# Optimization experiments

Hardware: AMD Instinct MI355X
Metric: run time of the kernel (lower is better)

Reference implementation:

```python
import jax, jax.numpy as jnp
import numpy as np

B, S, H, NH = 2, 2048, 2048, 16
HD = H // NH


def setup_inputs() -> dict:
    key = jax.random.key(0)
    ks = jax.random.split(key, 9)
    s = 1.0 / np.sqrt(H)
    return {
        "hidden_state": jax.random.normal(ks[0], (B, S, H), dtype=jnp.float32),
        "Wq": jax.random.normal(ks[1], (H, H), dtype=jnp.float32) * s,
        "bq": jnp.zeros((H,), dtype=jnp.float32),
        "Wk": jax.random.normal(ks[2], (H, H), dtype=jnp.float32) * s,
        "bk": jnp.zeros((H,), dtype=jnp.float32),
        "Wv": jax.random.normal(ks[3], (H, H), dtype=jnp.float32) * s,
        "bv": jnp.zeros((H,), dtype=jnp.float32),
        "Wo": jax.random.normal(ks[4], (H, H), dtype=jnp.float32) * s,
        "bo": jnp.zeros((H,), dtype=jnp.float32),
    }


def _split_heads(x):
    # [B,S,H] -> [B,NH,S,HD]
    b, s, _ = x.shape
    return x.reshape(b, s, NH, HD).transpose(0, 2, 1, 3)


def reference(hidden_state, Wq, bq, Wk, bk, Wv, bv, Wo, bo):
    q = _split_heads(hidden_state @ Wq.T + bq)
    k = _split_heads(hidden_state @ Wk.T + bk)
    v = _split_heads(hidden_state @ Wv.T + bv)
    scale = 1.0 / jnp.sqrt(jnp.array(HD, dtype=q.dtype))
    scores = jnp.einsum("bhqd,bhkd->bhqk", q, k) * scale
    attn = jax.nn.softmax(scores, axis=-1)
    out = jnp.einsum("bhqk,bhkd->bhqd", attn, v)  # [B,NH,S,HD]
    out = out.transpose(0, 2, 1, 3).reshape(hidden_state.shape[0], -1, H)
    return out @ Wo.T + bo
```

## Files before the change

### kernel.cpp

```cpp
#include <hip/hip_runtime.h>
#include <hip/hip_bf16.h>
#include <stdint.h>

#define B_ 2
#define S_ 2048
#define H_ 2048
#define NH_ 16
#define HD_ 128
#define M_ (B_*S_)

typedef __attribute__((ext_vector_type(8))) short short8_t;
typedef __attribute__((ext_vector_type(4))) float floatx4;
typedef __attribute__((ext_vector_type(16))) float floatx16;

__device__ __forceinline__ short f2bf(float f) {
  union { float f; uint32_t u; } x; x.f = f;
  const uint32_t u = x.u;
  return (short)((u + 0x7FFFu + ((u >> 16) & 1u)) >> 16);
}

__device__ __forceinline__ void gload_lds16(const void* g, void* l) {
  __builtin_amdgcn_global_load_lds(
      (const __attribute__((address_space(1))) void*)g,
      (__attribute__((address_space(3))) void*)l, 16, 0, 0);
}

__global__ __launch_bounds__(256)
void cast_all(const float* __restrict__ h,  const float* __restrict__ wq,
              const float* __restrict__ wk, const float* __restrict__ wv,
              const float* __restrict__ wo,
              short* __restrict__ hB,  short* __restrict__ wqB,
              short* __restrict__ wkB, short* __restrict__ wvB,
              short* __restrict__ woB) {
  const int blk = blockIdx.x;
  const float* src; short* dst; int off;
  if      (blk <  4096) { src = h;  dst = hB;  off = blk; }
  else if (blk <  6144) { src = wq; dst = wqB; off = blk - 4096; }
  else if (blk <  8192) { src = wk; dst = wkB; off = blk - 6144; }
  else if (blk < 10240) { src = wv; dst = wvB; off = blk - 8192; }
  else                  { src = wo; dst = woB; off = blk - 10240; }
  const int i = (off * 256 + threadIdx.x) * 8;
  typedef __attribute__((ext_vector_type(4))) float f4;
  const f4 a = *(const f4*)(src + i);
  const f4 b = *(const f4*)(src + i + 4);
  short8_t o;
  o[0] = f2bf(a[0]); o[1] = f2bf(a[1]); o[2] = f2bf(a[2]); o[3] = f2bf(a[3]);
  o[4] = f2bf(b[0]); o[5] = f2bf(b[1]); o[6] = f2bf(b[2]); o[7] = f2bf(b[3]);
  *(short8_t*)(dst + i) = o;
}

template<int MODE>
__device__ __forceinline__
void gemm_body(const short* __restrict__ A, const short* __restrict__ Bm,
               const float* __restrict__ bias, void* __restrict__ C,
               const int m0, const int n0, const int N, const int K) {
  __shared__ short As[128 * 64];
  __shared__ short Bs[128 * 64];
  const int tid = threadIdx.x;
  const int wv = tid >> 6, ln = tid & 63;
  const int lr = ln >> 4, lc = ln & 15;
  const int wm = (wv >> 1) * 64, wn = (wv & 1) * 64;
  const int srow = ln >> 3;
  const int sc   = (ln & 7) ^ srow;

  floatx4 acc[4][4] = {};
  const short* aP[4];
  const short* bP[4];
#pragma unroll
  for (int i = 0; i < 4; ++i)
    aP[i] = A + (size_t)(m0 + wv * 32 + i * 8 + srow) * K + sc * 8;
#pragma unroll
  for (int i = 0; i < 4; ++i)
    bP[i] = Bm + (size_t)(n0 + wv * 32 + i * 8 + srow) * K + sc * 8;
  const int sw = (lc & 7) << 3;

  for (int k0 = 0; k0 < K; k0 += 64) {
#pragma unroll
    for (int i = 0; i < 4; ++i)
      gload_lds16(aP[i] + k0, &As[(wv * 32 + i * 8) * 64]);
#pragma unroll
    for (int i = 0; i < 4; ++i)
      gload_lds16(bP[i] + k0, &Bs[(wv * 32 + i * 8) * 64]);
    __syncthreads();
#pragma unroll
    for (int ksq = 0; ksq < 2; ++ksq) {
      short8_t af[4], bf[4];
#pragma unroll
      for (int t = 0; t < 4; ++t)
        af[t] = *(const short8_t*)&As[(wm + t * 16 + lc) * 64 + ((ksq * 32 + lr * 8) ^ sw)];
#pragma unroll
      for (int t = 0; t < 4; ++t)
        bf[t] = *(const short8_t*)&Bs[(wn + t * 16 + lc) * 64 + ((ksq * 32 + lr * 8) ^ sw)];
#pragma unroll
      for (int i = 0; i < 4; ++i)
#pragma unroll
        for (int j = 0; j < 4; ++j)
          acc[i][j] = __builtin_amdgcn_mfma_f32_16x16x32_bf16(af[i], bf[j], acc[i][j], 0, 0, 0);
    }
    __syncthreads();
  }

#pragma unroll
  for (int i = 0; i < 4; ++i) {
#pragma unroll
    for (int j = 0; j < 4; ++j) {
      const int col = n0 + wn + j * 16 + lc;
      const float bv = bias[col];
#pragma unroll
      for (int r = 0; r < 4; ++r) {
        const int row = m0 + wm + i * 16 + lr * 4 + r;
        const float v = acc[i][j][r] + bv;
        if (MODE == 1) ((float*)C)[(size_t)row * N + col] = v;
        else           ((short*)C)[(size_t)row * N + col] = f2bf(v);
      }
    }
  }
}

__global__ __launch_bounds__(256)
void gemm_qkv(const short* __restrict__ A,
              const short* __restrict__ W0, const short* __restrict__ W1, const short* __restrict__ W2,
              const float* __restrict__ b0, const float* __restrict__ b1, const float* __restrict__ b2,
              short* __restrict__ C0, short* __restrict__ C1, short* __restrict__ C2) {
  const int sel = blockIdx.x >> 4;
  const short* Bm   = sel == 0 ? W0 : (sel == 1 ? W1 : W2);
  const float* bias = sel == 0 ? b0 : (sel == 1 ? b1 : b2);
  short* C          = sel == 0 ? C0 : (sel == 1 ? C1 : C2);
  gemm_body<0>(A, Bm, bias, C, blockIdx.y * 128, (blockIdx.x & 15) * 128, H_, H_);
}

__global__ __launch_bounds__(256)
void gemm_out(const short* __restrict__ A, const short* __restrict__ Bm,
              const float* __restrict__ bias, float* __restrict__ C) {
  gemm_body<1>(A, Bm, bias, C, blockIdx.y * 128, blockIdx.x * 128, H_, H_);
}

__global__ __launch_bounds__(256)
void arrange_v(const short* __restrict__ V, short* __restrict__ Vt) {
  __shared__ short T[64][72];
  const int b = blockIdx.z;
  const int s0 = blockIdx.x * 64, c0 = blockIdx.y * 64;
  const int t = threadIdx.x;
  const int r = t >> 3, c8 = (t & 7) * 8;
  const int kt = s0 >> 6;
#pragma unroll
  for (int p = 0; p < 2; ++p) {
    const int row = p * 32 + r;
    *(short8_t*)&T[row][c8] =
        *(const short8_t*)&V[(size_t)(b * S_ + s0 + row) * H_ + c0 + c8];
  }
  __syncthreads();
#pragma unroll
  for (int p = 0; p < 2; ++p) {
    const int row = p * 32 + r;
    const int gcol = c0 + row;
    const int hh = gcol >> 7, d = gcol & 127;
    short8_t o;
#pragma unroll
    for (int j = 0; j < 8; ++j) o[j] = T[c8 + j][row];
    const int chunk = (c8 >> 3) ^ (d & 7);
    *(short8_t*)&Vt[((((size_t)(b * 16 + hh) * 32 + kt) * 128 + d) << 6) + chunk * 8] = o;
  }
}

__global__ __launch_bounds__(256, 2)
void attention(const short* __restrict__ Q, const short* __restrict__ Kg,
               const short* __restrict__ Vt, short* __restrict__ O) {
  __shared__ short Ks[2][64 * 128];
  __shared__ short Vs[2][128 * 64];
  __shared__ float invLds[128];

  const int tid = threadIdx.x;
  const int wv = tid >> 6, ln = tid & 63;
  const int l32 = ln & 31, lh = ln >> 5;
  const int bh = blockIdx.y, b = bh >> 4, h = bh & 15;
  const int qw = blockIdx.x * 128 + wv * 32;

  const short* Qp  = Q  + ((size_t)(b * S_ + qw)) * H_ + h * HD_;
  const short* VtB = Vt + (size_t)bh * (S_ * HD_) + (size_t)wv * 2048 + ln * 8;

  const short* kp[4];
#pragma unroll
  for (int j = 0; j < 4; ++j) {
    const int key = wv * 16 + j * 4 + (ln >> 4);
    const int sc = (ln & 15) ^ (key & 7);
    kp[j] = Kg + (size_t)(b * S_ + key) * H_ + h * HD_ + sc * 8;
  }

  short8_t qf[8];
#pragma unroll
  for (int ksq = 0; ksq < 8; ++ksq)
    qf[ksq] = *(const short8_t*)&Qp[(size_t)l32 * H_ + ksq * 16 + lh * 8];

  floatx16 oacc[4] = {};
  float lsum = 0.f;
  const float csc = 0.08838834764831845f * 1.4426950408889634f;

#pragma unroll
  for (int j = 0; j < 4; ++j)
    gload_lds16(kp[j], &Ks[0][(wv * 16 + j * 4) * 128]);
#pragma unroll
  for (int j = 0; j < 4; ++j)
    gload_lds16(VtB + j * 512, &Vs[0][wv * 2048 + j * 512]);

  for (int kt = 0; kt < S_ / 64; ++kt) {
    const int cur = kt & 1;
    __syncthreads();

    if (kt + 1 < S_ / 64) {
      const size_t kadv = (size_t)(kt + 1) * 64 * H_;
#pragma unroll
      for (int j = 0; j < 4; ++j)
        gload_lds16(kp[j] + kadv, &Ks[cur ^ 1][(wv * 16 + j * 4) * 128]);
#pragma unroll
      for (int j = 0; j < 4; ++j)
        gload_lds16(VtB + (size_t)(kt + 1) * 8192 + j * 512, &Vs[cur ^ 1][wv * 2048 + j * 512]);
    }

    floatx16 sacc[2] = {};
#pragma unroll
    for (int kh = 0; kh < 2; ++kh) {
      const int key = kh * 32 + l32;
      const int swk = (key & 7) * 8;
#pragma unroll
      for (int ksq = 0; ksq < 8; ++ksq) {
        const short8_t kf =
            *(const short8_t*)&Ks[cur][key * 128 + (((ksq * 2 + lh) * 8) ^ swk)];
        sacc[kh] = __builtin_amdgcn_mfma_f32_32x32x16_bf16(kf, qf[ksq], sacc[kh], 0, 0, 0);
      }
    }

    int pfr[4][4];
#pragma unroll
    for (int kh = 0; kh < 2; ++kh) {
      uint32_t P[8];
#pragma unroll
      for (int i = 0; i < 8; ++i) {
        const uint32_t u0 = __float_as_uint(exp2f(sacc[kh][2 * i] * csc));
        const uint32_t u1 = __float_as_uint(exp2f(sacc[kh][2 * i + 1] * csc));
        lsum += __uint_as_float(u0 & 0xffff0000u) + __uint_as_float(u1 & 0xffff0000u);
        P[i] = (u0 >> 16) | (u1 & 0xffff0000u);
      }
#pragma unroll
      for (int t = 0; t < 2; ++t)
#pragma unroll
        for (int j = 0; j < 2; ++j) {
          const int a = (int)P[t * 4 + j], bb = (int)P[t * 4 + j + 2];
          const int as = __shfl_xor(a, 32), bs = __shfl_xor(bb, 32);
          pfr[kh * 2 + t][j]     = lh ? bs : a;
          pfr[kh * 2 + t][j + 2] = lh ? bb : as;
        }
    }

#pragma unroll
    for (int kf = 0; kf < 4; ++kf) {
      union { int i[4]; short8_t s; } pu;
#pragma unroll
      for (int j = 0; j < 4; ++j) pu.i[j] = pfr[kf][j];
#pragma unroll
      for (int dt = 0; dt < 4; ++dt) {
        const int d = dt * 32 + l32;
        const short8_t vf =
            *(const short8_t*)&Vs[cur][d * 64 + (((kf * 2 + lh) * 8) ^ ((d & 7) * 8))];
        oacc[dt] = __builtin_amdgcn_mfma_f32_32x32x16_bf16(pu.s, vf, oacc[dt], 0, 0, 0);
      }
    }
  }

  const float l = lsum + __shfl_xor(lsum, 32);
  invLds[wv * 32 + l32] = 1.0f / l;
  float inv[16];
#pragma unroll
  for (int r = 0; r < 16; ++r)
    inv[r] = invLds[wv * 32 + (r & 3) + 8 * (r >> 2) + 4 * lh];
  short* Op = O + ((size_t)(b * S_ + qw)) * H_ + h * HD_;
#pragma unroll
  for (int dt = 0; dt < 4; ++dt)
#pragma unroll
    for (int r = 0; r < 16; ++r) {
      const int rowl = (r & 3) + 8 * (r >> 2) + 4 * lh;
      Op[(size_t)rowl * H_ + dt * 32 + l32] = f2bf(oacc[dt][r] * inv[r]);
    }
}

extern "C" void kernel_launch(void* const* d_in, const int* in_sizes, int n_in,
                              void* d_out, int out_size, void* d_ws, size_t ws_size,
                              hipStream_t stream) {
  const float* hidden = (const float*)d_in[0];
  const float* Wq = (const float*)d_in[1];
  const float* bq = (const float*)d_in[2];
  const float* Wk = (const float*)d_in[3];
  const float* bk = (const float*)d_in[4];
  const float* Wv = (const float*)d_in[5];
  const float* bv = (const float*)d_in[6];
  const float* Wo = (const float*)d_in[7];
  const float* bo = (const float*)d_in[8];
  float* out = (float*)d_out;

  char* ws = (char*)d_ws;
  short* hB  = (short*)(ws);
  short* WqB = (short*)(ws + (16u << 20));
  short* WkB = (short*)(ws + (24u << 20));
  short* WvB = (short*)(ws + (32u << 20));
  short* WoB = (short*)(ws + (40u << 20));
  short* Qb  = (short*)(ws + (48u << 20));
  short* Kb  = (short*)(ws + (64u << 20));
  short* Vb  = (short*)(ws + (80u << 20));
  short* Vtb = (short*)(ws + (96u << 20));
  short* Ob  = (short*)(ws + (112u << 20));

  cast_all<<<12288, 256, 0, stream>>>(hidden, Wq, Wk, Wv, Wo, hB, WqB, WkB, WvB, WoB);

  gemm_qkv<<<dim3(48, M_ / 128), 256, 0, stream>>>(hB, WqB, WkB, WvB, bq, bk, bv, Qb, Kb, Vb);

  arrange_v<<<dim3(S_ / 64, H_ / 64, B_), 256, 0, stream>>>(Vb, Vtb);

  attention<<<dim3(S_ / 128, B_ * NH_), 256, 0, stream>>>(Qb, Kb, Vtb, Ob);

  gemm_out<<<dim3(H_ / 128, M_ / 128), 256, 0, stream>>>(Ob, WoB, bo, out);
}
```

Baseline: 404.0 us.

## Use 256x128 GEMM tiles with a 4-stage async LDS prefetch pipeline

Both projection GEMMs now use 512-thread blocks computing 256x128 output tiles instead of 256-thread 128x128 tiles. The K loop steps by 32 and rotates through a 4-deep ring of LDS buffers in dynamic shared memory, prefetching three stages ahead with direct global-to-LDS loads. Explicit vmcnt waits and raw barriers replace the full __syncthreads pairs, and the MFMA section runs at raised wave priority. The intent is to hide global load latency behind matrix math and improve operand reuse. In exchange it needs 96KB of LDS per block, which limits how many blocks fit per CU, and it relies on hand-placed wait counts that must match the issued load count.

```diff
diff --git a/kernel.cpp b/kernel.cpp
--- a/kernel.cpp
+++ b/kernel.cpp
@@ -51,54 +51,77 @@
 
 template<int MODE>
 __device__ __forceinline__
-void gemm_body(const short* __restrict__ A, const short* __restrict__ Bm,
-               const float* __restrict__ bias, void* __restrict__ C,
-               const int m0, const int n0, const int N, const int K) {
-  __shared__ short As[128 * 64];
-  __shared__ short Bs[128 * 64];
+void gemm_body256(const short* __restrict__ A, const short* __restrict__ Bm,
+                  const float* __restrict__ bias, void* __restrict__ C,
+                  const int m0, const int n0, const int N, const int K) {
+  extern __shared__ short lds[];
+  short* As = lds;
+  short* Bs = lds + 32768;
+
   const int tid = threadIdx.x;
-  const int wv = tid >> 6, ln = tid & 63;
-  const int lr = ln >> 4, lc = ln & 15;
-  const int wm = (wv >> 1) * 64, wn = (wv & 1) * 64;
-  const int srow = ln >> 3;
-  const int sc   = (ln & 7) ^ srow;
+  const int w  = tid >> 6, ln = tid & 63;
+  const int lr = ln >> 4,  lc = ln & 15;
+  const int wm = (w >> 1) << 6;
+  const int wn = (w & 1) << 6;
+
+  const int srr = ln >> 2;
+  const int sgc = (ln & 3) ^ ((ln >> 3) & 3);
+
+  const short* aSrc0 = A  + (size_t)(m0 + (w * 2 + 0) * 16 + srr) * K + sgc * 8;
+  const short* aSrc1 = A  + (size_t)(m0 + (w * 2 + 1) * 16 + srr) * K + sgc * 8;
+  const short* bSrc  = Bm + (size_t)(n0 +  w * 16          + srr) * K + sgc * 8;
+
+  const int aDst0 = (w * 2 + 0) * 512;
+  const int aDst1 = (w * 2 + 1) * 512;
+  const int bDst  =  w * 512;
+
+#define STAGE_(t_) do {                                      \
+    const int bq_ = (t_) & 3; const int ko_ = (t_) * 32;     \
+    gload_lds16(aSrc0 + ko_, &As[bq_ * 8192 + aDst0]);       \
+    gload_lds16(aSrc1 + ko_, &As[bq_ * 8192 + aDst1]);       \
+    gload_lds16(bSrc  + ko_, &Bs[bq_ * 4096 + bDst]);        \
+  } while (0)
+
+  STAGE_(0); STAGE_(1); STAGE_(2);
 
   floatx4 acc[4][4] = {};
-  const short* aP[4];
-  const short* bP[4];
-#pragma unroll
-  for (int i = 0; i < 4; ++i)
-    aP[i] = A + (size_t)(m0 + wv * 32 + i * 8 + srow) * K + sc * 8;
-#pragma unroll
-  for (int i = 0; i < 4; ++i)
-    bP[i] = Bm + (size_t)(n0 + wv * 32 + i * 8 + srow) * K + sc * 8;
-  const int sw = (lc & 7) << 3;
-
-  for (int k0 = 0; k0 < K; k0 += 64) {
+  const int swz = (lr ^ ((lc >> 1) & 3)) << 3;
+  const int aro = (wm + lc) * 32 + swz;
+  const int bro = (wn + lc) * 32 + swz;
+
+  asm volatile("s_waitcnt vmcnt(6)" ::: "memory");
+  __builtin_amdgcn_s_barrier();
+
+  const int NT = K >> 5;
+  for (int t = 0; t < NT; ++t) {
+    const int cb = t & 3;
+    short8_t af[4], bf[4];
 #pragma unroll
     for (int i = 0; i < 4; ++i)
-      gload_lds16(aP[i] + k0, &As[(wv * 32 + i * 8) * 64]);
+      af[i] = *(const short8_t*)&As[cb * 8192 + aro + i * 512];
+#pragma unroll
+    for (int j = 0; j < 4; ++j)
+      bf[j] = *(const short8_t*)&Bs[cb * 4096 + bro + j * 512];
+
+    if (t + 3 < NT) STAGE_(t + 3);
+
+    __builtin_amdgcn_s_barrier();
+    asm volatile("s_waitcnt lgkmcnt(0)" ::: "memory");
+    __builtin_amdgcn_sched_barrier(0);
+    __builtin_amdgcn_s_setprio(1);
 #pragma unroll
     for (int i = 0; i < 4; ++i)
-      gload_lds16(bP[i] + k0, &Bs[(wv * 32 + i * 8) * 64]);
-    __syncthreads();
-#pragma unroll
-    for (int ksq = 0; ksq < 2; ++ksq) {
-      short8_t af[4], bf[4];
-#pragma unroll
-      for (int t = 0; t < 4; ++t)
-        af[t] = *(const short8_t*)&As[(wm + t * 16 + lc) * 64 + ((ksq * 32 + lr * 8) ^ sw)];
-#pragma unroll
-      for (int t = 0; t < 4; ++t)
-        bf[t] = *(const short8_t*)&Bs[(wn + t * 16 + lc) * 64 + ((ksq * 32 + lr * 8) ^ sw)];
-#pragma unroll
-      for (int i = 0; i < 4; ++i)
-#pragma unroll
-        for (int j = 0; j < 4; ++j)
-          acc[i][j] = __builtin_amdgcn_mfma_f32_16x16x32_bf16(af[i], bf[j], acc[i][j], 0, 0, 0);
-    }
-    __syncthreads();
-  }
+#pragma unroll
+      for (int j = 0; j < 4; ++j)
+        acc[i][j] = __builtin_amdgcn_mfma_f32_16x16x32_bf16(af[i], bf[j], acc[i][j], 0, 0, 0);
+    __builtin_amdgcn_s_setprio(0);
+    __builtin_amdgcn_sched_barrier(0);
+    if (t < NT - 3)       asm volatile("s_waitcnt vmcnt(6)" ::: "memory");
+    else if (t == NT - 3) asm volatile("s_waitcnt vmcnt(3)" ::: "memory");
+    else if (t == NT - 2) asm volatile("s_waitcnt vmcnt(0)" ::: "memory");
+    __builtin_amdgcn_s_barrier();
+  }
+#undef STAGE_
 
 #pragma unroll
   for (int i = 0; i < 4; ++i) {
@@ -117,7 +140,7 @@
   }
 }
 
-__global__ __launch_bounds__(256)
+__global__ __launch_bounds__(512, 2)
 void gemm_qkv(const short* __restrict__ A,
               const short* __restrict__ W0, const short* __restrict__ W1, const short* __restrict__ W2,
               const float* __restrict__ b0, const float* __restrict__ b1, const float* __restrict__ b2,
@@ -126,13 +149,13 @@
   const short* Bm   = sel == 0 ? W0 : (sel == 1 ? W1 : W2);
   const float* bias = sel == 0 ? b0 : (sel == 1 ? b1 : b2);
   short* C          = sel == 0 ? C0 : (sel == 1 ? C1 : C2);
-  gemm_body<0>(A, Bm, bias, C, blockIdx.y * 128, (blockIdx.x & 15) * 128, H_, H_);
-}
-
-__global__ __launch_bounds__(256)
+  gemm_body256<0>(A, Bm, bias, C, blockIdx.y * 256, (blockIdx.x & 15) * 128, H_, H_);
+}
+
+__global__ __launch_bounds__(512, 2)
 void gemm_out(const short* __restrict__ A, const short* __restrict__ Bm,
               const float* __restrict__ bias, float* __restrict__ C) {
-  gemm_body<1>(A, Bm, bias, C, blockIdx.y * 128, blockIdx.x * 128, H_, H_);
+  gemm_body256<1>(A, Bm, bias, C, blockIdx.y * 256, blockIdx.x * 128, H_, H_);
 }
 
 __global__ __launch_bounds__(256)
@@ -309,13 +332,23 @@
   short* Vtb = (short*)(ws + (96u << 20));
   short* Ob  = (short*)(ws + (112u << 20));
 
+  constexpr int GEMM_LDS = (4 * 8192 + 4 * 4096) * 2;
+  static int lds_set = 0;
+  if (!lds_set) {
+    lds_set = 1;
+    (void)hipFuncSetAttribute((const void*)gemm_qkv,
+        hipFuncAttributeMaxDynamicSharedMemorySize, GEMM_LDS);
+    (void)hipFuncSetAttribute((const void*)gemm_out,
+        hipFuncAttributeMaxDynamicSharedMemorySize, GEMM_LDS);
+  }
+
   cast_all<<<12288, 256, 0, stream>>>(hidden, Wq, Wk, Wv, Wo, hB, WqB, WkB, WvB, WoB);
 
-  gemm_qkv<<<dim3(48, M_ / 128), 256, 0, stream>>>(hB, WqB, WkB, WvB, bq, bk, bv, Qb, Kb, Vb);
+  gemm_qkv<<<dim3(48, 16), 512, GEMM_LDS, stream>>>(hB, WqB, WkB, WvB, bq, bk, bv, Qb, Kb, Vb);
 
   arrange_v<<<dim3(S_ / 64, H_ / 64, B_), 256, 0, stream>>>(Vb, Vtb);
 
   attention<<<dim3(S_ / 128, B_ * NH_), 256, 0, stream>>>(Qb, Kb, Vtb, Ob);
 
-  gemm_out<<<dim3(H_ / 128, M_ / 128), 256, 0, stream>>>(Ob, WoB, bo, out);
-}
+  gemm_out<<<dim3(16, 16), 512, GEMM_LDS, stream>>>(Ob, WoB, bo, out);
+}
```

New measurement: 402.4 us. No clear change (-0.4%).
